# Kernel tuning notes

Measured on AMD Instinct MI355X. Metric: run time of the kernel, lower is better.

The kernel has to match this reference:

```python
import jax, jax.numpy as jnp
import numpy as np

B, N, C = 4, 32768, 3          # batch, proposals per sample, classes
PRE, POST = 4096, 512          # NMS_PRE_MAXSIZE, NMS_POST_MAXSIZE
THRESH = 0.7                   # NMS_THRESH


def setup_inputs() -> dict:
    key = jax.random.key(0)
    k1, k2, k3, k4 = jax.random.split(key, 4)
    # realistic 3D boxes: centers in a ~70m range, sizes 1-5m, heading in (-pi, pi)
    centers = jax.random.uniform(k1, (B, N, 3), minval=-35.0, maxval=35.0)
    sizes = jax.random.uniform(k2, (B, N, 3), minval=1.0, maxval=5.0)
    heading = jax.random.uniform(k3, (B, N, 1), minval=-np.pi, maxval=np.pi)
    batch_box_preds = jnp.concatenate([centers, sizes, heading], axis=-1)  # (B,N,7)
    batch_cls_preds = jax.random.normal(k4, (B, N, C))                     # (B,N,3)
    return {"batch_box_preds": batch_box_preds, "batch_cls_preds": batch_cls_preds}


def _bev_iou(boxes):
    # boxes: (K, 7) = (x, y, z, dx, dy, dz, ry); axis-aligned BEV IoU -> (K, K)
    x, y, dx, dy = boxes[:, 0], boxes[:, 1], boxes[:, 3], boxes[:, 4]
    x1, x2 = x - dx * 0.5, x + dx * 0.5
    y1, y2 = y - dy * 0.5, y + dy * 0.5
    iw = jnp.clip(jnp.minimum(x2[:, None], x2[None, :]) - jnp.maximum(x1[:, None], x1[None, :]), 0.0)
    ih = jnp.clip(jnp.minimum(y2[:, None], y2[None, :]) - jnp.maximum(y1[:, None], y1[None, :]), 0.0)
    inter = iw * ih
    area = dx * dy
    union = area[:, None] + area[None, :] - inter
    return inter / jnp.maximum(union, 1e-6)


def _nms_one(boxes, cls_preds):
    # boxes: (N, 7), cls_preds: (N, C)
    scores = jnp.max(cls_preds, axis=1)          # per-box max-class score
    labels = jnp.argmax(cls_preds, axis=1)
    top_scores, idx = jax.lax.top_k(scores, PRE)  # score-sorted candidates
    iou = _bev_iou(boxes[idx])                    # (PRE, PRE)
    ar = jnp.arange(PRE)

    def body(i, keep):
        # suppress later boxes overlapping a still-kept box i
        suppress = (iou[i] > THRESH) & keep[i] & (ar > i)
        return keep & (~suppress)

    keep = jax.lax.fori_loop(0, PRE, body, jnp.ones(PRE, dtype=bool))

    # take first POST kept (already score-ordered); pad with zeros like torch new_zeros buffers
    _, sel_local = jax.lax.top_k(jnp.where(keep, top_scores, -jnp.inf), POST)
    valid = keep[sel_local]
    sel = idx[sel_local]
    rois = jnp.where(valid[:, None], boxes[sel], 0.0)            # (POST, 7)
    roi_scores = jnp.where(valid, scores[sel], 0.0)              # (POST,)
    roi_labels = jnp.where(valid, labels[sel], 0) + 1            # (POST,), +1 as in proposal_layer
    return rois, roi_scores, roi_labels


def reference(batch_box_preds, batch_cls_preds):
    rois, roi_scores, roi_labels = jax.vmap(_nms_one)(batch_box_preds, batch_cls_preds)
    return rois, roi_scores, roi_labels
```

## Files before the change

kernel.cpp:

```cpp
#include <hip/hip_runtime.h>
#include <cstdint>
#include <cstddef>

#define BB 4
#define NN 32768
#define PRE 4096
#define POST 512
#define NW 64
#define PSEL 1024
#define PREF_CH 16
#define NBIN 4096
#define CEQ 32768

typedef unsigned long long u64;
typedef unsigned int u32;
typedef float f4u __attribute__((ext_vector_type(4), aligned(4)));

#define SW(i) ((i) ^ (((i) >> 4) & 15))

__device__ __forceinline__ u32 enc_f32(float f) {
  u32 u = __float_as_uint(f);
  u32 m = (u32)((int)u >> 31) | 0x80000000u;
  return u ^ m;
}
__device__ __forceinline__ float dec_f32(u32 e) {
  u32 u = (e & 0x80000000u) ? (e ^ 0x80000000u) : ~e;
  return __uint_as_float(u);
}

__global__ __launch_bounds__(256) void prep_kernel(
    const float* __restrict__ cls, float* __restrict__ scores,
    int* __restrict__ labels, u32* __restrict__ bhist) {
  int blk = blockIdx.x, b = blockIdx.y;
  int tid = threadIdx.x;
  __shared__ u32 lhist[NBIN];
  for (int i = tid; i < NBIN; i += 256) lhist[i] = 0;
  __syncthreads();

  const int E = blk * 2048 + tid * 8;
  const float4* cp4 = (const float4*)(cls + ((size_t)b * NN + E) * 3);
  float4 v0 = cp4[0], v1 = cp4[1], v2 = cp4[2], v3 = cp4[3], v4 = cp4[4], v5 = cp4[5];
  float fa[24] = {v0.x, v0.y, v0.z, v0.w, v1.x, v1.y, v1.z, v1.w,
                  v2.x, v2.y, v2.z, v2.w, v3.x, v3.y, v3.z, v3.w,
                  v4.x, v4.y, v4.z, v4.w, v5.x, v5.y, v5.z, v5.w};
  float sc8[8];
  int lb8[8];
#pragma unroll
  for (int k = 0; k < 8; ++k) {
    float c0 = fa[3 * k], c1 = fa[3 * k + 1], c2 = fa[3 * k + 2];
    float m = c0; int l = 0;
    if (c1 > m) { m = c1; l = 1; }
    if (c2 > m) { m = c2; l = 2; }
    sc8[k] = m;
    lb8[k] = l;
    atomicAdd(&lhist[enc_f32(m) >> 20], 1u);
  }
  float4* so = (float4*)(scores + (size_t)b * NN + E);
  so[0] = make_float4(sc8[0], sc8[1], sc8[2], sc8[3]);
  so[1] = make_float4(sc8[4], sc8[5], sc8[6], sc8[7]);
  int4* lo = (int4*)(labels + (size_t)b * NN + E);
  lo[0] = make_int4(lb8[0], lb8[1], lb8[2], lb8[3]);
  lo[1] = make_int4(lb8[4], lb8[5], lb8[6], lb8[7]);
  __syncthreads();
  u32* row = bhist + (size_t)(b * 16 + blk) * NBIN;
  for (int i = tid; i < NBIN; i += 256) row[i] = lhist[i];
}

__global__ __launch_bounds__(256) void pivot_kernel(
    const u32* __restrict__ bhist, int* __restrict__ st2, u32* __restrict__ gcnt) {
  int b = blockIdx.x, t = threadIdx.x;
  u32 sb[16];
#pragma unroll
  for (int j = 0; j < 16; ++j) {
    u32 s = 0;
#pragma unroll
    for (int k = 0; k < 16; ++k) s += bhist[(size_t)(b * 16 + k) * NBIN + t * 16 + j];
    sb[j] = s;
  }
  u32 T = 0;
#pragma unroll
  for (int j = 0; j < 16; ++j) T += sb[j];
  __shared__ u32 ssum[256];
  ssum[t] = T;
  __syncthreads();
  for (int off = 1; off < 256; off <<= 1) {
    u32 v = ssum[t];
    u32 a = (t + off < 256) ? ssum[t + off] : 0u;
    __syncthreads();
    ssum[t] = v + a;
    __syncthreads();
  }
  u32 cum = (t < 255) ? ssum[t + 1] : 0u;
  for (int j = 15; j >= 0; --j) {
    u32 incl = cum + sb[j];
    if (incl >= (u32)PSEL && cum < (u32)PSEL) {
      st2[b * 2 + 0] = t * 16 + j;
      st2[b * 2 + 1] = PSEL - (int)cum;
    }
    cum = incl;
  }
  if (t == 0) { gcnt[b * 2 + 0] = 0; gcnt[b * 2 + 1] = 0; }
}

__global__ __launch_bounds__(256) void compact_kernel(
    const float* __restrict__ scores, const int* __restrict__ st2,
    u32* __restrict__ gcnt, u64* __restrict__ cand, u64* __restrict__ ceq) {
  int blk = blockIdx.x, b = blockIdx.y;
  int tid = threadIdx.x, lane = tid & 63;
  const int E = blk * 2048 + tid * 8;
  const float4* s4 = (const float4*)(scores + (size_t)b * NN + E);
  float4 a = s4[0], c = s4[1];
  float fs[8] = {a.x, a.y, a.z, a.w, c.x, c.y, c.z, c.w};
  const u32 pb = (u32)st2[b * 2 + 0];
  u32 encs[8];
  u32 gbits = 0, ebits = 0;
  u32 gtl = 0, eql = 0;
#pragma unroll
  for (int k = 0; k < 8; ++k) {
    u32 u = enc_f32(fs[k]);
    encs[k] = u;
    u32 bin = u >> 20;
    if (bin > pb) { gbits |= 1u << k; gtl++; }
    else if (bin == pb) { ebits |= 1u << k; eql++; }
  }
  u64 pack = ((u64)gtl << 32) | eql;
#pragma unroll
  for (int off = 1; off < 64; off <<= 1) {
    u64 t = __shfl_up(pack, off, 64);
    if (lane >= off) pack += t;
  }
  u64 tot = __shfl(pack, 63, 64);
  u32 bg = 0, be = 0;
  if (lane == 63) {
    bg = atomicAdd(&gcnt[b * 2 + 0], (u32)(tot >> 32));
    be = atomicAdd(&gcnt[b * 2 + 1], (u32)(tot & 0xFFFFFFFFu));
  }
  bg = (u32)__shfl((int)bg, 63, 64);
  be = (u32)__shfl((int)be, 63, 64);
  int pg = (int)(bg + (u32)(pack >> 32) - gtl);
  int pe = (int)(be + (u32)(pack & 0xFFFFFFFFu) - eql);
#pragma unroll
  for (int k = 0; k < 8; ++k) {
    u64 key = ((u64)encs[k] << 32) | (u32)(~(u32)(E + k));
    if ((gbits >> k) & 1u) cand[(size_t)b * PSEL + (pg++)] = key;
    else if ((ebits >> k) & 1u) ceq[(size_t)b * CEQ + (pe++)] = key;
  }
}

__device__ __forceinline__ u64 hybrid_sort1024(u64 key, u64* sortbuf, int tid) {
#pragma unroll
  for (int k2 = 2; k2 <= 64; k2 <<= 1) {
    for (int j = k2 >> 1; j > 0; j >>= 1) {
      u64 o = __shfl_xor(key, j, 64);
      bool take_max = (((tid & k2) == 0) == ((tid & j) == 0));
      key = ((key > o) == take_max) ? key : o;
    }
  }
  for (int k2 = 128; k2 <= PSEL; k2 <<= 1) {
    for (int j = k2 >> 1; j >= 64; j >>= 1) {
      __syncthreads();
      sortbuf[tid] = key;
      __syncthreads();
      u64 o = sortbuf[tid ^ j];
      bool take_max = (((tid & k2) == 0) == ((tid & j) == 0));
      key = ((key > o) == take_max) ? key : o;
    }
    for (int j = 32; j > 0; j >>= 1) {
      u64 o = __shfl_xor(key, j, 64);
      bool take_max = (((tid & k2) == 0) == ((tid & j) == 0));
      key = ((key > o) == take_max) ? key : o;
    }
  }
  return key;
}

__global__ __launch_bounds__(1024) void sort1024_kernel(
    const float* __restrict__ boxes,
    const int* __restrict__ st2, const u32* __restrict__ gcnt,
    const u64* __restrict__ cand, const u64* __restrict__ ceq,
    int* __restrict__ top_idx, float* __restrict__ top_score,
    float* __restrict__ bx1, float* __restrict__ bx2,
    float* __restrict__ by1, float* __restrict__ by2, float* __restrict__ bar) {
  int b = blockIdx.x;
  int tid = threadIdx.x;
  __shared__ u64 sortbuf[PSEL];
  __shared__ u64 ebuf[PSEL];

  const int g = (int)gcnt[b * 2 + 0];
  const int m = (int)gcnt[b * 2 + 1];
  const int need = st2[b * 2 + 1];

  if (tid < g) ebuf[tid] = cand[(size_t)b * PSEL + tid];

  if (m <= PSEL) {
    u64 ek = (tid < m) ? ceq[(size_t)b * CEQ + tid] : 0ull;
    ek = hybrid_sort1024(ek, sortbuf, tid);
    if (tid < need) ebuf[g + tid] = ek;
  } else {
    const int qmax = (m + 1023) >> 10;
    for (int q = 0; q < qmax; ++q) {
      int i = q * 1024 + tid;
      u64 kk = (i < m) ? ceq[(size_t)b * CEQ + i] : 0ull;
      u32 rr = 0;
      for (int base = 0; base < m; base += 1024) {
        int cn = min(1024, m - base);
        __syncthreads();
        if (tid < cn) sortbuf[tid] = ceq[(size_t)b * CEQ + base + tid];
        __syncthreads();
        for (int j = 0; j < cn; ++j) rr += (sortbuf[j] > kk);
      }
      if (i < m && rr < (u32)need) ebuf[g + rr] = kk;
    }
  }
  __syncthreads();

  u64 key = ebuf[tid];
  key = hybrid_sort1024(key, sortbuf, tid);

  {
#pragma clang fp contract(off)
    u32 ue = (u32)(key >> 32);
    int e = (int)(~(u32)key);
    top_idx[b * PRE + tid] = e;
    top_score[b * PRE + tid] = dec_f32(ue);
    const float* bx = boxes + ((size_t)b * NN + e) * 7;
    f4u p0 = *(const f4u*)(bx);
    f4u p1 = *(const f4u*)(bx + 3);
    float x = p0.x, y = p0.y, dx = p0.w, dy = p1.y;
    float hx = dx * 0.5f, hy = dy * 0.5f;
    bx1[b * PRE + tid] = x - hx;
    bx2[b * PRE + tid] = x + hx;
    by1[b * PRE + tid] = y - hy;
    by2[b * PRE + tid] = y + hy;
    bar[b * PRE + tid] = dx * dy;
  }
}

template<int SELN, bool GATED>
__global__ __launch_bounds__(1024) void select_kernel_t(
    const float* __restrict__ scores, const float* __restrict__ boxes,
    const int* __restrict__ st_info,
    int* __restrict__ top_idx, float* __restrict__ top_score,
    float* __restrict__ bx1, float* __restrict__ bx2,
    float* __restrict__ by1, float* __restrict__ by2, float* __restrict__ bar) {
  int b = blockIdx.x;
  if (GATED && st_info[b * 2 + 0] >= POST) return;
  int tid = threadIdx.x;
  int wv = tid >> 6;
  const float* sc = scores + (size_t)b * NN;

  __shared__ u32 hist16[16][256];
  __shared__ u32 sA[256], sB[256];
  __shared__ u32 scanbuf[1024];
  __shared__ u64 sortbuf[SELN];
  __shared__ u32 sh_prefix;
  __shared__ int sh_rem;

  const int e0 = tid * 32;
  u32 encs[32];
  {
    const float4* sc4 = (const float4*)(sc + e0);
#pragma unroll
    for (int k = 0; k < 8; ++k) {
      float4 v = sc4[k];
      encs[k * 4 + 0] = enc_f32(v.x);
      encs[k * 4 + 1] = enc_f32(v.y);
      encs[k * 4 + 2] = enc_f32(v.z);
      encs[k * 4 + 3] = enc_f32(v.w);
    }
  }

  u32 prefix = 0, known = 0;
  int remaining = SELN;
  for (int shift = 24; shift >= 0; shift -= 8) {
    for (int k = tid; k < 16 * 256; k += 1024) ((u32*)hist16)[k] = 0;
    __syncthreads();
#pragma unroll
    for (int k = 0; k < 32; ++k) {
      u32 u = encs[k];
      if ((u & known) == prefix) atomicAdd(&hist16[wv][(u >> shift) & 255u], 1u);
    }
    __syncthreads();
    if (tid < 256) {
      u32 t = 0;
#pragma unroll
      for (int w2 = 0; w2 < 16; ++w2) t += hist16[w2][tid];
      sA[tid] = t;
    }
    __syncthreads();
    u32* src = sA; u32* dst = sB;
    for (int off = 1; off < 256; off <<= 1) {
      if (tid < 256) dst[tid] = src[tid] + ((tid + off < 256) ? src[tid + off] : 0u);
      __syncthreads();
      u32* tp = src; src = dst; dst = tp;
    }
    if (tid < 256) {
      u32 sv = src[tid];
      u32 svn = (tid < 255) ? src[tid + 1] : 0u;
      if (sv >= (u32)remaining && svn < (u32)remaining) {
        sh_prefix = prefix | ((u32)tid << shift);
        sh_rem = remaining - (int)svn;
      }
    }
    __syncthreads();
    prefix = sh_prefix;
    remaining = sh_rem;
    known |= (0xFFu << shift);
    __syncthreads();
  }
  const u32 pivot = prefix;

  int gtc = 0, eqc = 0;
#pragma unroll
  for (int k = 0; k < 32; ++k) {
    gtc += (encs[k] > pivot);
    eqc += (encs[k] == pivot);
  }
  scanbuf[tid] = ((u32)gtc << 16) | (u32)eqc;
  __syncthreads();
  for (int off = 1; off < 1024; off <<= 1) {
    u32 v = scanbuf[tid];
    u32 add = (tid >= off) ? scanbuf[tid - off] : 0u;
    __syncthreads();
    scanbuf[tid] = v + add;
    __syncthreads();
  }
  u32 incl = scanbuf[tid];
  u32 totpk = scanbuf[1023];
  const int cnt_gt = (int)(totpk >> 16);
  int gt_base = (int)(incl >> 16) - gtc;
  int eq_base = (int)(incl & 0xFFFFu) - eqc;
  int gs = 0, es = 0;
#pragma unroll
  for (int k = 0; k < 32; ++k) {
    u32 u = encs[k];
    int e = e0 + k;
    u64 key = ((u64)u << 32) | (u32)(~(u32)e);
    if (u > pivot) {
      sortbuf[SW(gt_base + gs)] = key; gs++;
    } else if (u == pivot) {
      int g = eq_base + (es++);
      if (g < remaining) sortbuf[SW(cnt_gt + g)] = key;
    }
  }
  __syncthreads();

  for (int k = 2; k <= SELN; k <<= 1) {
    for (int j = k >> 1; j > 0; j >>= 1) {
      for (int p = tid; p < SELN / 2; p += 1024) {
        int low = p & (j - 1);
        int i = ((p ^ low) << 1) | low;
        int ixj = i + j;
        u64 a = sortbuf[SW(i)], c = sortbuf[SW(ixj)];
        bool desc = ((i & k) == 0);
        if (desc ? (a < c) : (a > c)) { sortbuf[SW(i)] = c; sortbuf[SW(ixj)] = a; }
      }
      __syncthreads();
    }
  }
  {
#pragma clang fp contract(off)
    for (int s = tid; s < SELN; s += 1024) {
      u64 key = sortbuf[SW(s)];
      int e = (int)(~(u32)(key & 0xFFFFFFFFull));
      top_idx[b * PRE + s] = e;
      top_score[b * PRE + s] = sc[e];
      const float* bx = boxes + ((size_t)b * NN + e) * 7;
      float x = bx[0], y = bx[1], dx = bx[3], dy = bx[4];
      float hx = dx * 0.5f, hy = dy * 0.5f;
      bx1[b * PRE + s] = x - hx;
      bx2[b * PRE + s] = x + hx;
      by1[b * PRE + s] = y - hy;
      by2[b * PRE + s] = y + hy;
      bar[b * PRE + s] = dx * dy;
    }
  }
}

__device__ __forceinline__ void mask_tile(
    const float* __restrict__ bx1, const float* __restrict__ bx2,
    const float* __restrict__ by1, const float* __restrict__ by2,
    const float* __restrict__ bar, u64* __restrict__ mask,
    int b, int rb, int cb, int t) {
#pragma clang fp contract(off)
  int i = rb * 64 + t;
  int j0 = cb * 64 + t;
  float cx1 = bx1[b * PRE + j0], cx2 = bx2[b * PRE + j0];
  float cy1 = by1[b * PRE + j0], cy2 = by2[b * PRE + j0];
  float car = bar[b * PRE + j0];
  float ix1 = bx1[b * PRE + i], ix2 = bx2[b * PRE + i];
  float iy1 = by1[b * PRE + i], iy2 = by2[b * PRE + i];
  float ia = bar[b * PRE + i];
  u64 bits = 0ull;
  int jbase = cb * 64;
  for (int jj = 0; jj < 64; ++jj) {
    float jx1 = __shfl(cx1, jj, 64);
    float jx2 = __shfl(cx2, jj, 64);
    float jy1 = __shfl(cy1, jj, 64);
    float jy2 = __shfl(cy2, jj, 64);
    float jar = __shfl(car, jj, 64);
    if (jbase + jj > i) {
      float iw = fminf(ix2, jx2) - fmaxf(ix1, jx1);
      iw = fmaxf(iw, 0.0f);
      float ih = fminf(iy2, jy2) - fmaxf(iy1, jy1);
      ih = fmaxf(ih, 0.0f);
      float inter = iw * ih;
      float uni = ia + jar - inter;
      float iou = inter / fmaxf(uni, 1e-6f);
      if (iou > 0.7f) bits |= (1ull << jj);
    }
  }
  mask[((size_t)b * PRE + i) * NW + cb] = bits;
}

__global__ void mask_prefix_kernel(const float* __restrict__ bx1, const float* __restrict__ bx2,
                                   const float* __restrict__ by1, const float* __restrict__ by2,
                                   const float* __restrict__ bar, u64* __restrict__ mask) {
  int cb = blockIdx.x, rb = blockIdx.y, b = blockIdx.z;
  if (cb < rb) return;
  mask_tile(bx1, bx2, by1, by2, bar, mask, b, rb, cb, threadIdx.x);
}

__global__ __launch_bounds__(256) void mask_full_kernel(
    const float* __restrict__ bx1, const float* __restrict__ bx2,
    const float* __restrict__ by1, const float* __restrict__ by2,
    const float* __restrict__ bar, u64* __restrict__ mask,
    const int* __restrict__ st_info) {
  int b = blockIdx.y;
  if (st_info[b * 2 + 0] >= POST) return;
  int cb = blockIdx.x * 4 + (threadIdx.x >> 6);
  int t = threadIdx.x & 63;
  for (int rb = 0; rb <= cb; ++rb)
    mask_tile(bx1, bx2, by1, by2, bar, mask, b, rb, cb, t);
}

template<bool FULL>
__global__ __launch_bounds__(256) void nms_kernel_t(
    const u64* __restrict__ mask, u64* __restrict__ keep_words,
    int* __restrict__ st_info) {
  int b = blockIdx.x;
  if (FULL && st_info[b * 2 + 0] >= POST) return;
  int tid = threadIdx.x;
  int lane = tid & 63;
  int wv = tid >> 6;
  __shared__ u64 part[2][4][64];

  const u64* base = mask + (size_t)b * PRE * NW;
  u64 rem = 0ull, keepw = 0ull;
  int kept = 0;
  const int c1 = FULL ? NW : PREF_CH;

  int c = 0;
  while (c < c1) {
    u64 remc = __shfl(rem, c, 64);
    const u64* rowp = base + ((size_t)(c * 64 + wv * 16)) * NW + lane;
    u64 m[16];
#pragma unroll
    for (int k = 0; k < 16; ++k) m[k] = rowp[(size_t)k * NW];
    u64 dg = base[((size_t)(c * 64 + lane)) * NW + c];
    u64 nz = __ballot(dg != 0ull);
    while (nz) {
      int i2 = __builtin_ctzll(nz);
      nz &= nz - 1ull;
      u64 di = __shfl(dg, i2, 64);
      if (!((remc >> i2) & 1ull)) remc |= di;
    }
    u64 K = ~remc;
    if (lane == c) keepw = K;
    kept += __popcll(K);

    u32 kb = (u32)((K >> (wv * 16)) & 0xFFFFull);
    u64 acc = 0ull;
#pragma unroll
    for (int k = 0; k < 16; ++k)
      if ((kb >> k) & 1u) acc |= m[k];
    part[c & 1][wv][lane] = acc;
    __syncthreads();
    rem |= part[c & 1][0][lane] | part[c & 1][1][lane] |
           part[c & 1][2][lane] | part[c & 1][3][lane];
    ++c;
    if (kept >= POST) break;
  }

  if (wv == 0) {
    keep_words[b * 64 + lane] = keepw;
    if (!FULL && lane == 0) st_info[b * 2 + 0] = kept;
  }
}

__global__ __launch_bounds__(1024) void output_kernel(
    const u64* __restrict__ keep_words, const int* __restrict__ top_idx,
    const float* __restrict__ top_score, const int* __restrict__ labels,
    const float* __restrict__ boxes, float* __restrict__ out) {
  int b = blockIdx.x, tid = threadIdx.x;
  __shared__ u32 scanbuf[1024];
  __shared__ int sh_total;

  u64 w = keep_words[b * 64 + (tid >> 4)];
  u32 my4 = (u32)((w >> ((tid & 15) * 4)) & 0xFull);
  int cnt = __popc(my4);
  scanbuf[tid] = (u32)cnt;
  __syncthreads();
  for (int off = 1; off < 1024; off <<= 1) {
    u32 v = scanbuf[tid];
    u32 add = (tid >= off) ? scanbuf[tid - off] : 0u;
    __syncthreads();
    scanbuf[tid] = v + add;
    __syncthreads();
  }
  int base = (int)scanbuf[tid] - cnt;
  if (tid == 1023) sh_total = (int)scanbuf[1023];
  __syncthreads();
  int total = sh_total;

  float* rois = out;
  float* rsc = out + BB * POST * 7;
  float* rlb = rsc + BB * POST;

  int r = 0;
  for (int k = 0; k < 4; ++k) {
    if ((my4 >> k) & 1u) {
      int rank = base + (r++);
      if (rank < POST) {
        int i = tid * 4 + k;
        int idx = top_idx[b * PRE + i];
        const float* bx = boxes + ((size_t)b * NN + idx) * 7;
        float* ro = rois + ((size_t)b * POST + rank) * 7;
        for (int c = 0; c < 7; ++c) ro[c] = bx[c];
        rsc[b * POST + rank] = top_score[b * PRE + i];
        rlb[b * POST + rank] = (float)(labels[b * NN + idx] + 1);
      }
    }
  }
  for (int s = tid; s < POST; s += 1024) {
    if (s >= total) {
      float* ro = rois + ((size_t)b * POST + s) * 7;
      for (int c = 0; c < 7; ++c) ro[c] = 0.0f;
      rsc[b * POST + s] = 0.0f;
      rlb[b * POST + s] = 1.0f;
    }
  }
}

extern "C" void kernel_launch(void* const* d_in, const int* in_sizes, int n_in,
                              void* d_out, int out_size, void* d_ws, size_t ws_size,
                              hipStream_t stream) {
  const float* boxes = (const float*)d_in[0];
  const float* cls = (const float*)d_in[1];
  float* out = (float*)d_out;

  char* w = (char*)d_ws;
  float* scores = (float*)w;    w += (size_t)BB * NN * 4;
  int* labels = (int*)w;        w += (size_t)BB * NN * 4;
  int* top_idx = (int*)w;       w += (size_t)BB * PRE * 4;
  float* top_score = (float*)w; w += (size_t)BB * PRE * 4;
  float* bx1 = (float*)w;       w += (size_t)BB * PRE * 4;
  float* bx2 = (float*)w;       w += (size_t)BB * PRE * 4;
  float* by1 = (float*)w;       w += (size_t)BB * PRE * 4;
  float* by2 = (float*)w;       w += (size_t)BB * PRE * 4;
  float* bar = (float*)w;       w += (size_t)BB * PRE * 4;
  u64* mask = (u64*)w;          w += (size_t)BB * PRE * NW * 8;
  u64* keepw = (u64*)w;         w += (size_t)BB * 64 * 8;
  int* st_info = (int*)w;       w += (size_t)BB * 2 * 4;
  u32* bhist = (u32*)w;         w += (size_t)BB * 16 * NBIN * 4;
  u64* cand = (u64*)w;          w += (size_t)BB * PSEL * 8;
  u64* ceq = (u64*)w;           w += (size_t)BB * CEQ * 8;
  int* st2 = (int*)w;           w += (size_t)BB * 2 * 4;
  u32* gcnt = (u32*)w;          w += (size_t)BB * 2 * 4;

  prep_kernel<<<dim3(16, BB), 256, 0, stream>>>(cls, scores, labels, bhist);
  pivot_kernel<<<BB, 256, 0, stream>>>(bhist, st2, gcnt);
  compact_kernel<<<dim3(16, BB), 256, 0, stream>>>(scores, st2, gcnt, cand, ceq);
  sort1024_kernel<<<BB, 1024, 0, stream>>>(boxes, st2, gcnt, cand, ceq,
                                           top_idx, top_score, bx1, bx2, by1, by2, bar);
  mask_prefix_kernel<<<dim3(PREF_CH, PREF_CH, BB), 64, 0, stream>>>(
      bx1, bx2, by1, by2, bar, mask);
  nms_kernel_t<false><<<BB, 256, 0, stream>>>(mask, keepw, st_info);
  select_kernel_t<PRE, true><<<BB, 1024, 0, stream>>>(
      scores, boxes, st_info, top_idx, top_score, bx1, bx2, by1, by2, bar);
  mask_full_kernel<<<dim3(16, BB), 256, 0, stream>>>(
      bx1, bx2, by1, by2, bar, mask, st_info);
  nms_kernel_t<true><<<BB, 256, 0, stream>>>(mask, keepw, st_info);
  output_kernel<<<BB, 1024, 0, stream>>>(keepw, top_idx, top_score, labels, boxes, out);
}
```

Before: 124.2 us.

## Fuse pivot, compaction and sort into one kernel; slim prefix NMS loads

```diff
diff --git a/kernel.cpp b/kernel.cpp
--- a/kernel.cpp
+++ b/kernel.cpp
@@ -66,87 +66,6 @@
   for (int i = tid; i < NBIN; i += 256) row[i] = lhist[i];
 }
 
-__global__ __launch_bounds__(256) void pivot_kernel(
-    const u32* __restrict__ bhist, int* __restrict__ st2, u32* __restrict__ gcnt) {
-  int b = blockIdx.x, t = threadIdx.x;
-  u32 sb[16];
-#pragma unroll
-  for (int j = 0; j < 16; ++j) {
-    u32 s = 0;
-#pragma unroll
-    for (int k = 0; k < 16; ++k) s += bhist[(size_t)(b * 16 + k) * NBIN + t * 16 + j];
-    sb[j] = s;
-  }
-  u32 T = 0;
-#pragma unroll
-  for (int j = 0; j < 16; ++j) T += sb[j];
-  __shared__ u32 ssum[256];
-  ssum[t] = T;
-  __syncthreads();
-  for (int off = 1; off < 256; off <<= 1) {
-    u32 v = ssum[t];
-    u32 a = (t + off < 256) ? ssum[t + off] : 0u;
-    __syncthreads();
-    ssum[t] = v + a;
-    __syncthreads();
-  }
-  u32 cum = (t < 255) ? ssum[t + 1] : 0u;
-  for (int j = 15; j >= 0; --j) {
-    u32 incl = cum + sb[j];
-    if (incl >= (u32)PSEL && cum < (u32)PSEL) {
-      st2[b * 2 + 0] = t * 16 + j;
-      st2[b * 2 + 1] = PSEL - (int)cum;
-    }
-    cum = incl;
-  }
-  if (t == 0) { gcnt[b * 2 + 0] = 0; gcnt[b * 2 + 1] = 0; }
-}
-
-__global__ __launch_bounds__(256) void compact_kernel(
-    const float* __restrict__ scores, const int* __restrict__ st2,
-    u32* __restrict__ gcnt, u64* __restrict__ cand, u64* __restrict__ ceq) {
-  int blk = blockIdx.x, b = blockIdx.y;
-  int tid = threadIdx.x, lane = tid & 63;
-  const int E = blk * 2048 + tid * 8;
-  const float4* s4 = (const float4*)(scores + (size_t)b * NN + E);
-  float4 a = s4[0], c = s4[1];
-  float fs[8] = {a.x, a.y, a.z, a.w, c.x, c.y, c.z, c.w};
-  const u32 pb = (u32)st2[b * 2 + 0];
-  u32 encs[8];
-  u32 gbits = 0, ebits = 0;
-  u32 gtl = 0, eql = 0;
-#pragma unroll
-  for (int k = 0; k < 8; ++k) {
-    u32 u = enc_f32(fs[k]);
-    encs[k] = u;
-    u32 bin = u >> 20;
-    if (bin > pb) { gbits |= 1u << k; gtl++; }
-    else if (bin == pb) { ebits |= 1u << k; eql++; }
-  }
-  u64 pack = ((u64)gtl << 32) | eql;
-#pragma unroll
-  for (int off = 1; off < 64; off <<= 1) {
-    u64 t = __shfl_up(pack, off, 64);
-    if (lane >= off) pack += t;
-  }
-  u64 tot = __shfl(pack, 63, 64);
-  u32 bg = 0, be = 0;
-  if (lane == 63) {
-    bg = atomicAdd(&gcnt[b * 2 + 0], (u32)(tot >> 32));
-    be = atomicAdd(&gcnt[b * 2 + 1], (u32)(tot & 0xFFFFFFFFu));
-  }
-  bg = (u32)__shfl((int)bg, 63, 64);
-  be = (u32)__shfl((int)be, 63, 64);
-  int pg = (int)(bg + (u32)(pack >> 32) - gtl);
-  int pe = (int)(be + (u32)(pack & 0xFFFFFFFFu) - eql);
-#pragma unroll
-  for (int k = 0; k < 8; ++k) {
-    u64 key = ((u64)encs[k] << 32) | (u32)(~(u32)(E + k));
-    if ((gbits >> k) & 1u) cand[(size_t)b * PSEL + (pg++)] = key;
-    else if ((ebits >> k) & 1u) ceq[(size_t)b * CEQ + (pe++)] = key;
-  }
-}
-
 __device__ __forceinline__ u64 hybrid_sort1024(u64 key, u64* sortbuf, int tid) {
 #pragma unroll
   for (int k2 = 2; k2 <= 64; k2 <<= 1) {
@@ -174,23 +93,94 @@
   return key;
 }
 
-__global__ __launch_bounds__(1024) void sort1024_kernel(
-    const float* __restrict__ boxes,
-    const int* __restrict__ st2, const u32* __restrict__ gcnt,
-    const u64* __restrict__ cand, const u64* __restrict__ ceq,
+__global__ __launch_bounds__(1024) void selsort_kernel(
+    const float* __restrict__ scores, const float* __restrict__ boxes,
+    const u32* __restrict__ bhist, u64* __restrict__ ceq,
     int* __restrict__ top_idx, float* __restrict__ top_score,
     float* __restrict__ bx1, float* __restrict__ bx2,
     float* __restrict__ by1, float* __restrict__ by2, float* __restrict__ bar) {
   int b = blockIdx.x;
-  int tid = threadIdx.x;
+  int tid = threadIdx.x, lane = tid & 63;
   __shared__ u64 sortbuf[PSEL];
   __shared__ u64 ebuf[PSEL];
-
-  const int g = (int)gcnt[b * 2 + 0];
-  const int m = (int)gcnt[b * 2 + 1];
-  const int need = st2[b * 2 + 1];
-
-  if (tid < g) ebuf[tid] = cand[(size_t)b * PSEL + tid];
+  __shared__ u32 ssum[1024];
+  __shared__ int sh_pb, sh_need;
+  __shared__ u32 sh_cg, sh_cm;
+
+  u32 s0 = 0, s1 = 0, s2 = 0, s3 = 0;
+#pragma unroll
+  for (int k = 0; k < 16; ++k) {
+    const u32* hb = bhist + (size_t)(b * 16 + k) * NBIN + tid * 4;
+    s0 += hb[0]; s1 += hb[1]; s2 += hb[2]; s3 += hb[3];
+  }
+  ssum[tid] = s0 + s1 + s2 + s3;
+  __syncthreads();
+  for (int off = 1; off < 1024; off <<= 1) {
+    u32 v = ssum[tid];
+    u32 a = (tid + off < 1024) ? ssum[tid + off] : 0u;
+    __syncthreads();
+    ssum[tid] = v + a;
+    __syncthreads();
+  }
+  {
+    u32 cum = (tid < 1023) ? ssum[tid + 1] : 0u;
+    u32 incl;
+    incl = cum + s3; if (incl >= (u32)PSEL && cum < (u32)PSEL) { sh_pb = tid * 4 + 3; sh_need = PSEL - (int)cum; } cum = incl;
+    incl = cum + s2; if (incl >= (u32)PSEL && cum < (u32)PSEL) { sh_pb = tid * 4 + 2; sh_need = PSEL - (int)cum; } cum = incl;
+    incl = cum + s1; if (incl >= (u32)PSEL && cum < (u32)PSEL) { sh_pb = tid * 4 + 1; sh_need = PSEL - (int)cum; } cum = incl;
+    incl = cum + s0; if (incl >= (u32)PSEL && cum < (u32)PSEL) { sh_pb = tid * 4 + 0; sh_need = PSEL - (int)cum; } cum = incl;
+  }
+  if (tid == 0) { sh_cg = 0; sh_cm = 0; }
+  __syncthreads();
+  const u32 pb = (u32)sh_pb;
+
+  u32 encs[32];
+  {
+    const float4* sc4 = (const float4*)(scores + (size_t)b * NN + tid * 32);
+#pragma unroll
+    for (int k = 0; k < 8; ++k) {
+      float4 v = sc4[k];
+      encs[k * 4 + 0] = enc_f32(v.x);
+      encs[k * 4 + 1] = enc_f32(v.y);
+      encs[k * 4 + 2] = enc_f32(v.z);
+      encs[k * 4 + 3] = enc_f32(v.w);
+    }
+  }
+  u32 gtl = 0, eql = 0;
+#pragma unroll
+  for (int k = 0; k < 32; ++k) {
+    u32 bin = encs[k] >> 20;
+    gtl += (bin > pb);
+    eql += (bin == pb);
+  }
+  u64 pack = ((u64)gtl << 32) | eql;
+#pragma unroll
+  for (int off = 1; off < 64; off <<= 1) {
+    u64 t = __shfl_up(pack, off, 64);
+    if (lane >= off) pack += t;
+  }
+  u64 tot = __shfl(pack, 63, 64);
+  u32 bg = 0, be = 0;
+  if (lane == 63) {
+    bg = atomicAdd(&sh_cg, (u32)(tot >> 32));
+    be = atomicAdd(&sh_cm, (u32)(tot & 0xFFFFFFFFu));
+  }
+  bg = (u32)__shfl((int)bg, 63, 64);
+  be = (u32)__shfl((int)be, 63, 64);
+  int pg = (int)(bg + (u32)(pack >> 32) - gtl);
+  int pe = (int)(be + (u32)(pack & 0xFFFFFFFFu) - eql);
+#pragma unroll
+  for (int k = 0; k < 32; ++k) {
+    u32 bin = encs[k] >> 20;
+    u64 key = ((u64)encs[k] << 32) | (u32)(~(u32)(tid * 32 + k));
+    if (bin > pb) ebuf[pg++] = key;
+    else if (bin == pb) ceq[(size_t)b * CEQ + (pe++)] = key;
+  }
+  __syncthreads();
+
+  const int g = (int)sh_cg;
+  const int m = (int)sh_cm;
+  const int need = sh_need;
 
   if (m <= PSEL) {
     u64 ek = (tid < m) ? ceq[(size_t)b * CEQ + tid] : 0ull;
@@ -202,10 +192,10 @@
       int i = q * 1024 + tid;
       u64 kk = (i < m) ? ceq[(size_t)b * CEQ + i] : 0ull;
       u32 rr = 0;
-      for (int base = 0; base < m; base += 1024) {
-        int cn = min(1024, m - base);
+      for (int base2 = 0; base2 < m; base2 += 1024) {
+        int cn = min(1024, m - base2);
         __syncthreads();
-        if (tid < cn) sortbuf[tid] = ceq[(size_t)b * CEQ + base + tid];
+        if (tid < cn) sortbuf[tid] = ceq[(size_t)b * CEQ + base2 + tid];
         __syncthreads();
         for (int j = 0; j < cn; ++j) rr += (sortbuf[j] > kk);
       }
@@ -443,43 +433,81 @@
   int tid = threadIdx.x;
   int lane = tid & 63;
   int wv = tid >> 6;
-  __shared__ u64 part[2][4][64];
 
   const u64* base = mask + (size_t)b * PRE * NW;
   u64 rem = 0ull, keepw = 0ull;
   int kept = 0;
-  const int c1 = FULL ? NW : PREF_CH;
-
   int c = 0;
-  while (c < c1) {
-    u64 remc = __shfl(rem, c, 64);
-    const u64* rowp = base + ((size_t)(c * 64 + wv * 16)) * NW + lane;
-    u64 m[16];
-#pragma unroll
-    for (int k = 0; k < 16; ++k) m[k] = rowp[(size_t)k * NW];
-    u64 dg = base[((size_t)(c * 64 + lane)) * NW + c];
-    u64 nz = __ballot(dg != 0ull);
-    while (nz) {
-      int i2 = __builtin_ctzll(nz);
-      nz &= nz - 1ull;
-      u64 di = __shfl(dg, i2, 64);
-      if (!((remc >> i2) & 1ull)) remc |= di;
-    }
-    u64 K = ~remc;
-    if (lane == c) keepw = K;
-    kept += __popcll(K);
-
-    u32 kb = (u32)((K >> (wv * 16)) & 0xFFFFull);
-    u64 acc = 0ull;
-#pragma unroll
-    for (int k = 0; k < 16; ++k)
-      if ((kb >> k) & 1u) acc |= m[k];
-    part[c & 1][wv][lane] = acc;
-    __syncthreads();
-    rem |= part[c & 1][0][lane] | part[c & 1][1][lane] |
-           part[c & 1][2][lane] | part[c & 1][3][lane];
-    ++c;
-    if (kept >= POST) break;
+
+  if constexpr (!FULL) {
+    __shared__ u64 part[2][4][16];
+    const int g16 = lane >> 4;
+    const int w = lane & 15;
+    while (c < PREF_CH) {
+      u64 remc = __shfl(rem, c, 64);
+      const u64* rowb = base + ((size_t)(c * 64 + wv * 16)) * NW + w;
+      u64 m0 = rowb[(size_t)(0 + g16) * NW];
+      u64 m1 = rowb[(size_t)(4 + g16) * NW];
+      u64 m2 = rowb[(size_t)(8 + g16) * NW];
+      u64 m3 = rowb[(size_t)(12 + g16) * NW];
+      u64 dg = base[((size_t)(c * 64 + lane)) * NW + c];
+      u64 nz = __ballot(dg != 0ull);
+      while (nz) {
+        int i2 = __builtin_ctzll(nz);
+        nz &= nz - 1ull;
+        u64 di = __shfl(dg, i2, 64);
+        if (!((remc >> i2) & 1ull)) remc |= di;
+      }
+      u64 K = ~remc;
+      if (lane == c) keepw = K;
+      kept += __popcll(K);
+
+      u64 acc = 0ull;
+      if ((K >> (wv * 16 + 0 + g16)) & 1ull) acc |= m0;
+      if ((K >> (wv * 16 + 4 + g16)) & 1ull) acc |= m1;
+      if ((K >> (wv * 16 + 8 + g16)) & 1ull) acc |= m2;
+      if ((K >> (wv * 16 + 12 + g16)) & 1ull) acc |= m3;
+      acc |= __shfl_xor(acc, 16, 64);
+      acc |= __shfl_xor(acc, 32, 64);
+      if (g16 == 0) part[c & 1][wv][w] = acc;
+      __syncthreads();
+      rem |= part[c & 1][0][w] | part[c & 1][1][w] |
+             part[c & 1][2][w] | part[c & 1][3][w];
+      ++c;
+      if (kept >= POST) break;
+    }
+  } else {
+    __shared__ u64 part[2][4][64];
+    while (c < NW) {
+      u64 remc = __shfl(rem, c, 64);
+      const u64* rowp = base + ((size_t)(c * 64 + wv * 16)) * NW + lane;
+      u64 m[16];
+#pragma unroll
+      for (int k = 0; k < 16; ++k) m[k] = rowp[(size_t)k * NW];
+      u64 dg = base[((size_t)(c * 64 + lane)) * NW + c];
+      u64 nz = __ballot(dg != 0ull);
+      while (nz) {
+        int i2 = __builtin_ctzll(nz);
+        nz &= nz - 1ull;
+        u64 di = __shfl(dg, i2, 64);
+        if (!((remc >> i2) & 1ull)) remc |= di;
+      }
+      u64 K = ~remc;
+      if (lane == c) keepw = K;
+      kept += __popcll(K);
+
+      u32 kb = (u32)((K >> (wv * 16)) & 0xFFFFull);
+      u64 acc = 0ull;
+#pragma unroll
+      for (int k = 0; k < 16; ++k)
+        if ((kb >> k) & 1u) acc |= m[k];
+      part[c & 1][wv][lane] = acc;
+      __syncthreads();
+      rem |= part[c & 1][0][lane] | part[c & 1][1][lane] |
+             part[c & 1][2][lane] | part[c & 1][3][lane];
+      ++c;
+      if (kept >= POST) break;
+    }
   }
 
   if (wv == 0) {
@@ -563,16 +591,11 @@
   u64* keepw = (u64*)w;         w += (size_t)BB * 64 * 8;
   int* st_info = (int*)w;       w += (size_t)BB * 2 * 4;
   u32* bhist = (u32*)w;         w += (size_t)BB * 16 * NBIN * 4;
-  u64* cand = (u64*)w;          w += (size_t)BB * PSEL * 8;
   u64* ceq = (u64*)w;           w += (size_t)BB * CEQ * 8;
-  int* st2 = (int*)w;           w += (size_t)BB * 2 * 4;
-  u32* gcnt = (u32*)w;          w += (size_t)BB * 2 * 4;
 
   prep_kernel<<<dim3(16, BB), 256, 0, stream>>>(cls, scores, labels, bhist);
-  pivot_kernel<<<BB, 256, 0, stream>>>(bhist, st2, gcnt);
-  compact_kernel<<<dim3(16, BB), 256, 0, stream>>>(scores, st2, gcnt, cand, ceq);
-  sort1024_kernel<<<BB, 1024, 0, stream>>>(boxes, st2, gcnt, cand, ceq,
-                                           top_idx, top_score, bx1, bx2, by1, by2, bar);
+  selsort_kernel<<<BB, 1024, 0, stream>>>(scores, boxes, bhist, ceq,
+                                          top_idx, top_score, bx1, bx2, by1, by2, bar);
   mask_prefix_kernel<<<dim3(PREF_CH, PREF_CH, BB), 64, 0, stream>>>(
       bx1, bx2, by1, by2, bar, mask);
   nms_kernel_t<false><<<BB, 256, 0, stream>>>(mask, keepw, st_info);
```

Result: faster. 115.3 us (-7.2%).
